# Performance work log

Measured on AMD Instinct MI355X. Metric: run time of the kernel, lower is better.

Reference implementation:

```python
import jax, jax.numpy as jnp
import numpy as np

N_NODES = 50000


def _gcn_layer(x, src, dst, W, b, n_nodes):
    # x: [N, Cin] -> linear -> [N, Cout]
    h = x @ W.T + b
    # degree over destination (col) index, including self loops
    deg = jax.ops.segment_sum(jnp.ones(src.shape[0], dtype=x.dtype), dst,
                              num_segments=n_nodes)
    dinv = jnp.where(deg > 0, deg ** -0.5, jnp.zeros((), x.dtype))
    norm = dinv[src] * dinv[dst]                      # [E]
    msg = h[src] * norm[:, None]                      # gather + scale
    return jax.ops.segment_sum(msg, dst, num_segments=n_nodes)  # scatter-add


def setup_inputs() -> dict:
    key = jax.random.key(0)
    k1, k2, k3, k4, k5, k6 = jax.random.split(key, 6)
    num_features = 128
    hidden_dim = 128
    n_edges = 1_600_000
    x = jax.random.normal(k1, (N_NODES, num_features), dtype=jnp.float32)
    edge_index = jax.random.randint(k2, (2, n_edges), 0, N_NODES, dtype=jnp.int64)
    bound1 = 1.0 / np.sqrt(num_features)
    W1 = jax.random.uniform(k3, (hidden_dim, num_features), jnp.float32, -bound1, bound1)
    b1 = jax.random.uniform(k4, (hidden_dim,), jnp.float32, -bound1, bound1)
    bound2 = 1.0 / np.sqrt(hidden_dim)
    W2 = jax.random.uniform(k5, (hidden_dim, hidden_dim), jnp.float32, -bound2, bound2)
    b2 = jax.random.uniform(k6, (hidden_dim,), jnp.float32, -bound2, bound2)
    return {"x": x, "edge_index": edge_index, "W1": W1, "b1": b1, "W2": W2, "b2": b2}


def reference(x, edge_index, W1, b1, W2, b2):
    n_nodes = x.shape[0]
    # add_self_loops: append (i, i) for every node
    loops = jnp.arange(n_nodes, dtype=edge_index.dtype)
    src = jnp.concatenate([edge_index[0], loops])
    dst = jnp.concatenate([edge_index[1], loops])
    h = _gcn_layer(x, src, dst, W1, b1, n_nodes)
    h = jax.nn.relu(h)
    # dropout is identity in eval mode (deterministic reference)
    out = _gcn_layer(h, src, dst, W2, b2, n_nodes)
    return out
```

## Files before the change

kernel.cpp:

```cpp
#include <hip/hip_runtime.h>


static constexpr int F = 128;
static constexpr int NR = 128;
static constexpr int CH = 4096;
static constexpr int CAP = 4608;
static constexpr int RMAX = 512;

typedef __attribute__((ext_vector_type(8))) short bf16x8;
typedef __attribute__((ext_vector_type(4))) float f32x4;
typedef __attribute__((ext_vector_type(4))) unsigned short u16x4;

__device__ __forceinline__ unsigned f2b(float x) {
  unsigned u = __float_as_uint(x);
  return (u + 0x7fffu + ((u >> 16) & 1u)) >> 16;
}
__device__ __forceinline__ float b_lo(unsigned u) {
  return __uint_as_float(u << 16);
}
__device__ __forceinline__ float b_hi(unsigned u) {
  return __uint_as_float(u & 0xffff0000u);
}
__device__ __forceinline__ float b16f(unsigned short v) {
  return __uint_as_float(((unsigned)v) << 16);
}

__global__ void k_initcur(int* __restrict__ gcur, int R) {
  int i = blockIdx.x * blockDim.x + threadIdx.x;
  if (i < R) gcur[i] = i * CAP;
}

__global__ __launch_bounds__(256) void k_part(const int* __restrict__ src,
                                              const int* __restrict__ dst,
                                              int E, int R,
                                              int* __restrict__ gcur,
                                              unsigned* __restrict__ rsorted) {
  __shared__ int h[RMAX];
  __shared__ int cur[RMAX];
  for (int i = threadIdx.x; i < R; i += 256) h[i] = 0;
  __syncthreads();
  const int e0 = blockIdx.x * CH;
  const int e1 = min(e0 + CH, E);
  for (int i = e0 + threadIdx.x; i < e1; i += 256)
    atomicAdd(&h[dst[i] >> 7], 1);
  __syncthreads();
  for (int i = threadIdx.x; i < R; i += 256)
    cur[i] = h[i] ? atomicAdd(&gcur[i], h[i]) : 0;
  __syncthreads();
  for (int i = e0 + threadIdx.x; i < e1; i += 256) {
    const int d = dst[i];
    const int s = src[i];
    const int pos = atomicAdd(&cur[d >> 7], 1);
    rsorted[pos] = ((unsigned)(d & (NR - 1)) << 16) | (unsigned)s;
  }
}

__global__ __launch_bounds__(256) void k_fillR(
    const unsigned* __restrict__ rsorted, const int* __restrict__ gcur,
    int N, int* __restrict__ rowptr, int* __restrict__ rowend,
    float* __restrict__ dinv, unsigned short* __restrict__ csr) {
  __shared__ int cnt[NR];
  __shared__ int sc[NR];
  __shared__ int cur[NR];
  const int r = blockIdx.x;
  const int tid = threadIdx.x;
  const int b = r * CAP;
  const int e = gcur[r];
  if (tid < NR) cnt[tid] = 0;
  __syncthreads();
  for (int i = b + tid; i < e; i += 256)
    atomicAdd(&cnt[rsorted[i] >> 16], 1);
  __syncthreads();
  if (tid < NR) sc[tid] = cnt[tid];
  __syncthreads();
#pragma unroll
  for (int off = 1; off < NR; off <<= 1) {
    int a = (tid < NR && tid >= off) ? sc[tid - off] : 0;
    __syncthreads();
    if (tid < NR) sc[tid] += a;
    __syncthreads();
  }
  if (tid < NR) {
    const int excl = sc[tid] - cnt[tid];
    cur[tid] = excl;
    const int node = r * NR + tid;
    if (node < N) {
      rowptr[node] = b + excl;
      rowend[node] = b + excl + cnt[tid];
      dinv[node] = rsqrtf((float)(cnt[tid] + 1));
    }
  }
  __syncthreads();
  for (int i = b + tid; i < e; i += 256) {
    const unsigned v = rsorted[i];
    const int pos = b + atomicAdd(&cur[v >> 16], 1);
    csr[pos] = (unsigned short)(v & 0xFFFFu);
  }
}

__global__ __launch_bounds__(256) void k_splitW(const float* __restrict__ W,
                                                unsigned short* __restrict__ hi,
                                                unsigned short* __restrict__ lo) {
  const int i = blockIdx.x * 256 + threadIdx.x;
  const int j = i & 7;
  const int lane = (i >> 3) & 63;
  const int f = (i >> 9) & 7;
  const int t = i >> 12;
  const int col = f * 16 + (lane & 15);
  const int k = t * 32 + ((j & 4) << 2) + 4 * (lane >> 4) + (j & 3);
  const float x = W[col * F + k];
  const unsigned h = f2b(x);
  hi[i] = (unsigned short)h;
  lo[i] = (unsigned short)f2b(x - __uint_as_float(h << 16));
}

__global__ __launch_bounds__(256) void k_splitA(const float* __restrict__ A,
                                                unsigned short* __restrict__ hi,
                                                unsigned short* __restrict__ lo,
                                                int n4) {
  const int i = blockIdx.x * 256 + threadIdx.x;
  if (i >= n4) return;
  const float4 v = *(const float4*)(A + (size_t)i * 4);
  u16x4 h, l;
  unsigned u;
  u = f2b(v.x); h[0] = (unsigned short)u; l[0] = (unsigned short)f2b(v.x - __uint_as_float(u << 16));
  u = f2b(v.y); h[1] = (unsigned short)u; l[1] = (unsigned short)f2b(v.y - __uint_as_float(u << 16));
  u = f2b(v.z); h[2] = (unsigned short)u; l[2] = (unsigned short)f2b(v.z - __uint_as_float(u << 16));
  u = f2b(v.w); h[3] = (unsigned short)u; l[3] = (unsigned short)f2b(v.w - __uint_as_float(u << 16));
  *(u16x4*)(hi + (size_t)i * 4) = h;
  *(u16x4*)(lo + (size_t)i * 4) = l;
}

__global__ __launch_bounds__(256) void k_gemm_mfma(
    const unsigned short* __restrict__ Ahi, const unsigned short* __restrict__ Alo,
    const unsigned short* __restrict__ Whi, const unsigned short* __restrict__ Wlo,
    const float* __restrict__ bias, const float* __restrict__ dinv,
    unsigned short* __restrict__ hout, int n) {
  const int wid = threadIdx.x >> 6;
  const int lane = threadIdx.x & 63;
  const int r = lane & 15;
  const int g = lane >> 4;
  const int m0 = blockIdx.x * 64 + wid * 16;
  const int arow = m0 + r;

  f32x4 acc[8];
#pragma unroll
  for (int f = 0; f < 8; ++f) acc[f] = (f32x4){0.f, 0.f, 0.f, 0.f};

#pragma unroll
  for (int t = 0; t < 4; ++t) {
    bf16x8 bhi[8], blo[8];
#pragma unroll
    for (int f = 0; f < 8; ++f) {
      const size_t base = (((size_t)t * 8 + f) * 64 + lane) * 8;
      bhi[f] = *(const bf16x8*)(Whi + base);
      blo[f] = *(const bf16x8*)(Wlo + base);
    }
    const int kt = t * 32;
    bf16x8 ahi = (bf16x8){0, 0, 0, 0, 0, 0, 0, 0};
    bf16x8 alo = (bf16x8){0, 0, 0, 0, 0, 0, 0, 0};
    if (arow < n) {
      const size_t ab = (size_t)arow * F + kt + 4 * g;
      const u16x4 h0 = *(const u16x4*)(Ahi + ab);
      const u16x4 h1 = *(const u16x4*)(Ahi + ab + 16);
      const u16x4 l0 = *(const u16x4*)(Alo + ab);
      const u16x4 l1 = *(const u16x4*)(Alo + ab + 16);
      ahi[0] = (short)h0[0]; ahi[1] = (short)h0[1]; ahi[2] = (short)h0[2]; ahi[3] = (short)h0[3];
      ahi[4] = (short)h1[0]; ahi[5] = (short)h1[1]; ahi[6] = (short)h1[2]; ahi[7] = (short)h1[3];
      alo[0] = (short)l0[0]; alo[1] = (short)l0[1]; alo[2] = (short)l0[2]; alo[3] = (short)l0[3];
      alo[4] = (short)l1[0]; alo[5] = (short)l1[1]; alo[6] = (short)l1[2]; alo[7] = (short)l1[3];
    }
#pragma unroll
    for (int f = 0; f < 8; ++f) {
      acc[f] = __builtin_amdgcn_mfma_f32_16x16x32_bf16(ahi, bhi[f], acc[f], 0, 0, 0);
      acc[f] = __builtin_amdgcn_mfma_f32_16x16x32_bf16(ahi, blo[f], acc[f], 0, 0, 0);
      acc[f] = __builtin_amdgcn_mfma_f32_16x16x32_bf16(alo, bhi[f], acc[f], 0, 0, 0);
    }
  }

  int orow[4];
  float dv[4];
#pragma unroll
  for (int j = 0; j < 4; ++j) {
    orow[j] = m0 + 4 * g + j;
    dv[j] = (orow[j] < n) ? dinv[orow[j]] : 0.f;
  }
#pragma unroll
  for (int f = 0; f < 8; ++f) {
    const int col = f * 16 + r;
    const float bv = bias[col];
#pragma unroll
    for (int j = 0; j < 4; ++j) {
      if (orow[j] < n)
        hout[(size_t)orow[j] * F + col] = (unsigned short)f2b((acc[f][j] + bv) * dv[j]);
    }
  }
}

template <int MODE>
__global__ __launch_bounds__(256) void k_pull(
    const int* __restrict__ rowptr, const int* __restrict__ rowend,
    const unsigned short* __restrict__ csr, const uint2* __restrict__ h,
    const float* __restrict__ dinv, unsigned short* __restrict__ ahi,
    unsigned short* __restrict__ alo, float* __restrict__ fout, int n) {
  const int wid = (blockIdx.x * blockDim.x + threadIdx.x) >> 6;
  if (wid >= n) return;
  const int lane = threadIdx.x & 63;
  const int half = lane >> 5;
  const int l32 = lane & 31;
  const int beg = rowptr[wid];
  const int end = rowend[wid];

  float4 acc = make_float4(0.f, 0.f, 0.f, 0.f);
  if (half == 0) {
    const uint2 u = h[(size_t)wid * 32 + l32];
    acc.x = b_lo(u.x); acc.y = b_hi(u.x);
    acc.z = b_lo(u.y); acc.w = b_hi(u.y);
  }

  int k = beg + half;
  for (; k + 6 < end; k += 8) {
    const int s0 = __builtin_nontemporal_load(csr + k);
    const int s1 = __builtin_nontemporal_load(csr + k + 2);
    const int s2 = __builtin_nontemporal_load(csr + k + 4);
    const int s3 = __builtin_nontemporal_load(csr + k + 6);
    const uint2 u0 = h[(size_t)s0 * 32 + l32];
    const uint2 u1 = h[(size_t)s1 * 32 + l32];
    const uint2 u2 = h[(size_t)s2 * 32 + l32];
    const uint2 u3 = h[(size_t)s3 * 32 + l32];
    acc.x += b_lo(u0.x) + b_lo(u1.x) + b_lo(u2.x) + b_lo(u3.x);
    acc.y += b_hi(u0.x) + b_hi(u1.x) + b_hi(u2.x) + b_hi(u3.x);
    acc.z += b_lo(u0.y) + b_lo(u1.y) + b_lo(u2.y) + b_lo(u3.y);
    acc.w += b_hi(u0.y) + b_hi(u1.y) + b_hi(u2.y) + b_hi(u3.y);
  }
  for (; k < end; k += 2) {
    const uint2 u = h[(size_t)__builtin_nontemporal_load(csr + k) * 32 + l32];
    acc.x += b_lo(u.x);
    acc.y += b_hi(u.x);
    acc.z += b_lo(u.y);
    acc.w += b_hi(u.y);
  }

  acc.x += __shfl_xor(acc.x, 32, 64);
  acc.y += __shfl_xor(acc.y, 32, 64);
  acc.z += __shfl_xor(acc.z, 32, 64);
  acc.w += __shfl_xor(acc.w, 32, 64);

  if (half == 0) {
    const float dv = dinv[wid];
    float rx = acc.x * dv;
    float ry = acc.y * dv;
    float rz = acc.z * dv;
    float rw = acc.w * dv;
    if (MODE == 0) {
      rx = fmaxf(rx, 0.f);
      ry = fmaxf(ry, 0.f);
      rz = fmaxf(rz, 0.f);
      rw = fmaxf(rw, 0.f);
      u16x4 hv, lv;
      unsigned u;
      u = f2b(rx); hv[0] = (unsigned short)u; lv[0] = (unsigned short)f2b(rx - __uint_as_float(u << 16));
      u = f2b(ry); hv[1] = (unsigned short)u; lv[1] = (unsigned short)f2b(ry - __uint_as_float(u << 16));
      u = f2b(rz); hv[2] = (unsigned short)u; lv[2] = (unsigned short)f2b(rz - __uint_as_float(u << 16));
      u = f2b(rw); hv[3] = (unsigned short)u; lv[3] = (unsigned short)f2b(rw - __uint_as_float(u << 16));
      *(u16x4*)(ahi + (size_t)wid * F + l32 * 4) = hv;
      *(u16x4*)(alo + (size_t)wid * F + l32 * 4) = lv;
    } else {
      float* po = fout + (size_t)wid * F + l32 * 4;
      __builtin_nontemporal_store(rx, po);
      __builtin_nontemporal_store(ry, po + 1);
      __builtin_nontemporal_store(rz, po + 2);
      __builtin_nontemporal_store(rw, po + 3);
    }
  }
}

extern "C" void kernel_launch(void* const* d_in, const int* in_sizes, int n_in,
                              void* d_out, int out_size, void* d_ws, size_t ws_size,
                              hipStream_t stream) {
  const float* x  = (const float*)d_in[0];
  const int*   ei = (const int*)d_in[1];
  const float* W1 = (const float*)d_in[2];
  const float* b1 = (const float*)d_in[3];
  const float* W2 = (const float*)d_in[4];
  const float* b2 = (const float*)d_in[5];

  const int N = in_sizes[0] / F;
  const int E = in_sizes[1] / 2;
  const int* src = ei;
  const int* dst = ei + E;
  const int R = (N + NR - 1) / NR;
  const int C = (E + CH - 1) / CH;

  char* ws = (char*)d_ws;
  int*            gcur    = (int*)(ws + (8u << 10));
  float*          dinv    = (float*)(ws + (16u << 10));
  int*            rowptr  = (int*)(ws + (256u << 10));
  int*            rowend  = (int*)(ws + (512u << 10));
  unsigned short* Whi1    = (unsigned short*)(ws + (768u << 10));
  unsigned short* Wlo1    = (unsigned short*)(ws + (800u << 10));
  unsigned short* Whi2    = (unsigned short*)(ws + (832u << 10));
  unsigned short* Wlo2    = (unsigned short*)(ws + (864u << 10));
  unsigned*       rsorted = (unsigned*)(ws + (1u << 20));
  unsigned short* csr     = (unsigned short*)(ws + (9u << 20));
  unsigned short* hbuf    = (unsigned short*)(ws + (16u << 20));
  unsigned short* Ahi     = (unsigned short*)(ws + (32u << 20));
  unsigned short* Alo     = (unsigned short*)(ws + (45u << 20));
  float*          out     = (float*)d_out;

  const int B = 256;
  const int gemmBlocks = (N + 63) / 64;
  const int pullBlocks = (N * 64 + B - 1) / B;
  const int splitBlocks = (N * F / 4 + B - 1) / B;

  k_initcur<<<(R + 255) / 256, B, 0, stream>>>(gcur, R);
  k_part<<<C, B, 0, stream>>>(src, dst, E, R, gcur, rsorted);
  k_fillR<<<R, B, 0, stream>>>(rsorted, gcur, N, rowptr, rowend, dinv, csr);
  k_splitW<<<64, B, 0, stream>>>(W1, Whi1, Wlo1);
  k_splitW<<<64, B, 0, stream>>>(W2, Whi2, Wlo2);
  k_splitA<<<splitBlocks, B, 0, stream>>>(x, Ahi, Alo, N * F / 4);

  k_gemm_mfma<<<gemmBlocks, B, 0, stream>>>(Ahi, Alo, Whi1, Wlo1, b1, dinv,
                                            hbuf, N);
  k_pull<0><<<pullBlocks, B, 0, stream>>>(rowptr, rowend, csr,
                                          (const uint2*)hbuf, dinv, Ahi, Alo,
                                          nullptr, N);

  k_gemm_mfma<<<gemmBlocks, B, 0, stream>>>(Ahi, Alo, Whi2, Wlo2, b2, dinv,
                                            hbuf, N);
  k_pull<1><<<pullBlocks, B, 0, stream>>>(rowptr, rowend, csr,
                                          (const uint2*)hbuf, dinv, nullptr,
                                          nullptr, out, N);
}
```

Baseline: 226.0 us.

## Split pull aggregation into feature halves with XCD-aware block mapping

The pull kernel now handles each node's 128 features in two halves of 64, each in a separate block. Block ids are remapped so that blocks sharing a feature half land on the same group of XCDs, which shrinks the gathered working set each L2 sees to half the feature table. Each lane now issues 4-byte loads instead of 8-byte ones, doubling the number of waves and CSR index reads. Nontemporal hints on the CSR loads and output stores were also dropped.

```diff
diff --git a/kernel.cpp b/kernel.cpp
--- a/kernel.cpp
+++ b/kernel.cpp
@@ -20,9 +20,6 @@
 }
 __device__ __forceinline__ float b_hi(unsigned u) {
   return __uint_as_float(u & 0xffff0000u);
-}
-__device__ __forceinline__ float b16f(unsigned short v) {
-  return __uint_as_float(((unsigned)v) << 16);
 }
 
 __global__ void k_initcur(int* __restrict__ gcur, int R) {
@@ -200,77 +197,70 @@
 template <int MODE>
 __global__ __launch_bounds__(256) void k_pull(
     const int* __restrict__ rowptr, const int* __restrict__ rowend,
-    const unsigned short* __restrict__ csr, const uint2* __restrict__ h,
+    const unsigned short* __restrict__ csr, const unsigned* __restrict__ hb,
     const float* __restrict__ dinv, unsigned short* __restrict__ ahi,
     unsigned short* __restrict__ alo, float* __restrict__ fout, int n) {
-  const int wid = (blockIdx.x * blockDim.x + threadIdx.x) >> 6;
-  if (wid >= n) return;
+  const int b = blockIdx.x;
+  const int hf = (b & 7) >> 2;
+  const int g = ((b >> 3) << 2) | (b & 3);
+  const int node = g * 4 + (threadIdx.x >> 6);
+  if (node >= n) return;
   const int lane = threadIdx.x & 63;
   const int half = lane >> 5;
   const int l32 = lane & 31;
-  const int beg = rowptr[wid];
-  const int end = rowend[wid];
-
-  float4 acc = make_float4(0.f, 0.f, 0.f, 0.f);
+  const unsigned* __restrict__ hq = hb + hf * 32;
+
+  const int beg = rowptr[node];
+  const int end = rowend[node];
+
+  float2 acc = make_float2(0.f, 0.f);
   if (half == 0) {
-    const uint2 u = h[(size_t)wid * 32 + l32];
-    acc.x = b_lo(u.x); acc.y = b_hi(u.x);
-    acc.z = b_lo(u.y); acc.w = b_hi(u.y);
+    const unsigned u = hq[(size_t)node * 64 + l32];
+    acc.x = b_lo(u);
+    acc.y = b_hi(u);
   }
 
   int k = beg + half;
   for (; k + 6 < end; k += 8) {
-    const int s0 = __builtin_nontemporal_load(csr + k);
-    const int s1 = __builtin_nontemporal_load(csr + k + 2);
-    const int s2 = __builtin_nontemporal_load(csr + k + 4);
-    const int s3 = __builtin_nontemporal_load(csr + k + 6);
-    const uint2 u0 = h[(size_t)s0 * 32 + l32];
-    const uint2 u1 = h[(size_t)s1 * 32 + l32];
-    const uint2 u2 = h[(size_t)s2 * 32 + l32];
-    const uint2 u3 = h[(size_t)s3 * 32 + l32];
-    acc.x += b_lo(u0.x) + b_lo(u1.x) + b_lo(u2.x) + b_lo(u3.x);
-    acc.y += b_hi(u0.x) + b_hi(u1.x) + b_hi(u2.x) + b_hi(u3.x);
-    acc.z += b_lo(u0.y) + b_lo(u1.y) + b_lo(u2.y) + b_lo(u3.y);
-    acc.w += b_hi(u0.y) + b_hi(u1.y) + b_hi(u2.y) + b_hi(u3.y);
+    const int s0 = csr[k];
+    const int s1 = csr[k + 2];
+    const int s2 = csr[k + 4];
+    const int s3 = csr[k + 6];
+    const unsigned u0 = hq[(size_t)s0 * 64 + l32];
+    const unsigned u1 = hq[(size_t)s1 * 64 + l32];
+    const unsigned u2 = hq[(size_t)s2 * 64 + l32];
+    const unsigned u3 = hq[(size_t)s3 * 64 + l32];
+    acc.x += b_lo(u0) + b_lo(u1) + b_lo(u2) + b_lo(u3);
+    acc.y += b_hi(u0) + b_hi(u1) + b_hi(u2) + b_hi(u3);
   }
   for (; k < end; k += 2) {
-    const uint2 u = h[(size_t)__builtin_nontemporal_load(csr + k) * 32 + l32];
-    acc.x += b_lo(u.x);
-    acc.y += b_hi(u.x);
-    acc.z += b_lo(u.y);
-    acc.w += b_hi(u.y);
+    const unsigned u = hq[(size_t)csr[k] * 64 + l32];
+    acc.x += b_lo(u);
+    acc.y += b_hi(u);
   }
 
   acc.x += __shfl_xor(acc.x, 32, 64);
   acc.y += __shfl_xor(acc.y, 32, 64);
-  acc.z += __shfl_xor(acc.z, 32, 64);
-  acc.w += __shfl_xor(acc.w, 32, 64);
 
   if (half == 0) {
-    const float dv = dinv[wid];
+    const float dv = dinv[node];
     float rx = acc.x * dv;
     float ry = acc.y * dv;
-    float rz = acc.z * dv;
-    float rw = acc.w * dv;
     if (MODE == 0) {
       rx = fmaxf(rx, 0.f);
       ry = fmaxf(ry, 0.f);
-      rz = fmaxf(rz, 0.f);
-      rw = fmaxf(rw, 0.f);
-      u16x4 hv, lv;
+      const size_t o = (size_t)node * F + hf * 64 + l32 * 2;
+      unsigned uh, ul;
       unsigned u;
-      u = f2b(rx); hv[0] = (unsigned short)u; lv[0] = (unsigned short)f2b(rx - __uint_as_float(u << 16));
-      u = f2b(ry); hv[1] = (unsigned short)u; lv[1] = (unsigned short)f2b(ry - __uint_as_float(u << 16));
-      u = f2b(rz); hv[2] = (unsigned short)u; lv[2] = (unsigned short)f2b(rz - __uint_as_float(u << 16));
-      u = f2b(rw); hv[3] = (unsigned short)u; lv[3] = (unsigned short)f2b(rw - __uint_as_float(u << 16));
-      *(u16x4*)(ahi + (size_t)wid * F + l32 * 4) = hv;
-      *(u16x4*)(alo + (size_t)wid * F + l32 * 4) = lv;
+      u = f2b(rx); uh = u;       ul = f2b(rx - __uint_as_float(u << 16));
+      u = f2b(ry); uh |= u << 16; ul |= f2b(ry - __uint_as_float(u << 16)) << 16;
+      *(unsigned*)(ahi + o) = uh;
+      *(unsigned*)(alo + o) = ul;
     } else {
-      float* po = fout + (size_t)wid * F + l32 * 4;
-      __builtin_nontemporal_store(rx, po);
-      __builtin_nontemporal_store(ry, po + 1);
-      __builtin_nontemporal_store(rz, po + 2);
-      __builtin_nontemporal_store(rw, po + 3);
+      float2 rv;
+      rv.x = rx;
+      rv.y = ry;
+      *(float2*)(fout + (size_t)node * F + hf * 64 + l32 * 2) = rv;
     }
   }
 }
@@ -310,7 +300,8 @@
 
   const int B = 256;
   const int gemmBlocks = (N + 63) / 64;
-  const int pullBlocks = (N * 64 + B - 1) / B;
+  const int groups = (N + 3) / 4;
+  const int pullBlocks = 8 * ((groups + 3) / 4);
   const int splitBlocks = (N * F / 4 + B - 1) / B;
 
   k_initcur<<<(R + 255) / 256, B, 0, stream>>>(gcur, R);
@@ -323,12 +314,12 @@
   k_gemm_mfma<<<gemmBlocks, B, 0, stream>>>(Ahi, Alo, Whi1, Wlo1, b1, dinv,
                                             hbuf, N);
   k_pull<0><<<pullBlocks, B, 0, stream>>>(rowptr, rowend, csr,
-                                          (const uint2*)hbuf, dinv, Ahi, Alo,
-                                          nullptr, N);
+                                          (const unsigned*)hbuf, dinv, Ahi,
+                                          Alo, nullptr, N);
 
   k_gemm_mfma<<<gemmBlocks, B, 0, stream>>>(Ahi, Alo, Whi2, Wlo2, b2, dinv,
                                             hbuf, N);
   k_pull<1><<<pullBlocks, B, 0, stream>>>(rowptr, rowend, csr,
-                                          (const uint2*)hbuf, dinv, nullptr,
+                                          (const unsigned*)hbuf, dinv, nullptr,
                                           nullptr, out, N);
 }
```

Measured after the change: 248.3 us. +9.9%, slower.
